# Kernel optimization log

Hardware: AMD Instinct MI355X
Metric: run time of the kernel (lower is better)

Reference implementation:

```python
import jax, jax.numpy as jnp
import numpy as np

B, S, D, L = 64, 512, 768, 2


def setup_inputs() -> dict:
    key = jax.random.key(0)
    ks = jax.random.split(key, 8)
    sc = 1.0 / np.sqrt(D)
    sequence_output = jax.random.normal(ks[0], (B, S, D), dtype=jnp.float32)
    sot_positions = jax.random.randint(ks[1], (B, S), 0, 2, dtype=jnp.int32)
    # guarantee every sample has at least one selected token (torch nonzero-gather assumes this)
    sot_positions = sot_positions.at[:, 0].set(1)
    W_ih = jax.random.uniform(ks[2], (3 * D, D), jnp.float32, -sc, sc)
    W_hh = jax.random.uniform(ks[3], (3 * D, D), jnp.float32, -sc, sc)
    b_ih = jax.random.uniform(ks[4], (3 * D,), jnp.float32, -sc, sc)
    b_hh = jax.random.uniform(ks[5], (3 * D,), jnp.float32, -sc, sc)
    W_cls = jax.random.uniform(ks[6], (L, D), jnp.float32, -sc, sc)
    b_cls = jax.random.uniform(ks[7], (L,), jnp.float32, -sc, sc)
    return {"sequence_output": sequence_output, "sot_positions": sot_positions,
            "W_ih": W_ih, "W_hh": W_hh, "b_ih": b_ih, "b_hh": b_hh,
            "W_cls": W_cls, "b_cls": b_cls}


def _masked_gru_last(seq, mask, W_ih, W_hh, b_ih, b_hh):
    """Equivalent to: per sample, gather tokens where mask!=0, run a 1-layer GRU
    over that subsequence, return the final hidden state. Vectorized as a scan
    over time that freezes the hidden state at non-selected positions."""
    # precompute input projections for all timesteps: [B,S,3D]
    x_proj = jnp.einsum('bsd,ed->bse', seq, W_ih) + b_ih
    xs = (jnp.swapaxes(x_proj, 0, 1), jnp.swapaxes(mask, 0, 1))  # time-major
    h0 = jnp.zeros((seq.shape[0], W_hh.shape[1]), seq.dtype)

    def step(h, inp):
        xp, m = inp  # xp: [B,3D], m: [B]
        hp = h @ W_hh.T + b_hh  # [B,3D]
        xr, xz, xn = jnp.split(xp, 3, axis=-1)
        hr, hz, hn = jnp.split(hp, 3, axis=-1)
        r = jax.nn.sigmoid(xr + hr)
        z = jax.nn.sigmoid(xz + hz)
        n = jnp.tanh(xn + r * hn)
        h_new = (1.0 - z) * n + z * h
        h = jnp.where((m != 0)[:, None], h_new, h)
        return h, None

    h_last, _ = jax.lax.scan(step, h0, xs)
    return h_last  # [B,D]


def reference(sequence_output, sot_positions, W_ih, W_hh, b_ih, b_hh, W_cls, b_cls):
    match_vec = _masked_gru_last(sequence_output, sot_positions, W_ih, W_hh, b_ih, b_hh)
    # dropout is identity at eval time
    logits = match_vec @ W_cls.T + b_cls  # [B,L]
    return jax.nn.softmax(logits, axis=1)
```

## Files before the change

### kernel.cpp

```cpp
#include <hip/hip_runtime.h>
#include <hip/hip_bf16.h>


#define NB 64
#define NS 512
#define ND 768
#define TD 2304
#define NM 24

typedef __attribute__((ext_vector_type(4))) float f32x4;
typedef __attribute__((ext_vector_type(8))) short bf16x8;
typedef __attribute__((ext_vector_type(4))) unsigned int u32x4;

__device__ inline unsigned short f2bf(float f) {
  union { float f; unsigned u; } a; a.f = f;
  unsigned r = a.u + 0x7fff + ((a.u >> 16) & 1);
  return (unsigned short)(r >> 16);
}
__device__ inline float bf2f(unsigned short s) {
  union { unsigned u; float f; } a; a.u = ((unsigned)s) << 16;
  return a.f;
}

__device__ inline void load2_flag(const int* p0, const int* p1, int& a, int& b) {
  asm volatile("global_load_dword %0, %2, off sc0 sc1\n\t"
               "global_load_dword %1, %3, off sc0 sc1\n\t"
               "s_waitcnt vmcnt(0)"
               : "=&v"(a), "=&v"(b) : "v"(p0), "v"(p1) : "memory");
}
__device__ inline void store_flag(int* p, int v) {
  asm volatile("global_store_dword %0, %1, off sc0 sc1"
               :: "v"(p), "v"(v) : "memory");
}
__device__ inline void store_h16(void* p, u32x4 v) {
  asm volatile("global_store_dwordx4 %0, %1, off sc0 sc1"
               :: "v"(p), "v"(v) : "memory");
}
__device__ inline void load2_h16(const void* p0, const void* p1,
                                 u32x4& a, u32x4& b) {
  asm volatile("global_load_dwordx4 %0, %2, off sc0 sc1\n\t"
               "global_load_dwordx4 %1, %3, off sc0 sc1\n\t"
               "s_waitcnt vmcnt(0)"
               : "=&v"(a), "=&v"(b) : "v"(p0), "v"(p1) : "memory");
}
__device__ inline void waitcnt_vm0() {
  asm volatile("s_waitcnt vmcnt(0)" ::: "memory");
}

__global__ void cvt_f32_bf16(const float* __restrict__ in,
                             unsigned short* __restrict__ out, int n) {
  int i = (blockIdx.x * blockDim.x + threadIdx.x) * 4;
  int stride = gridDim.x * blockDim.x * 4;
  for (; i < n; i += stride) {
    float4 v = *(const float4*)(in + i);
    ushort4 o;
    o.x = f2bf(v.x); o.y = f2bf(v.y); o.z = f2bf(v.z); o.w = f2bf(v.w);
    *(ushort4*)(out + i) = o;
  }
}

__global__ void compact_pos(const int* __restrict__ sot,
                            int* __restrict__ pos, int* __restrict__ ctrl) {
  int b = blockIdx.x, t = threadIdx.x;
  int m = (sot[b * NS + t] != 0) ? 1 : 0;
  unsigned long long ball = __ballot(m);
  int wid = t >> 6, lane = t & 63;
  __shared__ int wcnt[8];
  int prefix = __popcll(ball & ((1ull << lane) - 1ull));
  if (lane == 63) wcnt[wid] = __popcll(ball);
  __syncthreads();
  int base = 0;
  for (int w = 0; w < wid; ++w) base += wcnt[w];
  if (m) pos[b * NS + base + prefix] = t;
  if (t == 511) {
    int total = base + wcnt[7];
    ctrl[b] = total;
    atomicMax(&ctrl[64], total);
  }
}

#define BM 128
#define BN 256
__global__ __launch_bounds__(256) void gemm_xg(
    const float* __restrict__ seq,
    const int* __restrict__ pos,
    const int* __restrict__ ctrl,
    const unsigned short* __restrict__ Bg,
    const float* __restrict__ bias,
    unsigned short* __restrict__ C) {
  const int cntmax = ctrl[64];
  const int m0 = blockIdx.x * BM;
  if (m0 >= cntmax * 64) return;
  const int n0 = blockIdx.y * BN;
  __shared__ unsigned short lA[BM * 64];
  __shared__ unsigned short lB[BN * 64];
  const int tid = threadIdx.x;
  const int wid = tid >> 6, lane = tid & 63;
  const int wm = (wid & 1) * 64, wn = (wid >> 1) * 128;

  f32x4 acc[4][8];
#pragma unroll
  for (int i = 0; i < 4; ++i)
#pragma unroll
    for (int j = 0; j < 8; ++j) { f32x4 z = {0.f,0.f,0.f,0.f}; acc[i][j] = z; }

  for (int kt = 0; kt < 12; ++kt) {
    __syncthreads();
#pragma unroll
    for (int c = 0; c < 4; ++c) {
      int idx = c * 256 + tid;
      int r = idx >> 3, ch = idx & 7;
      int gm = m0 + r, ks = gm >> 6, ss = gm & 63;
      float4 v0 = {0,0,0,0}, v1 = {0,0,0,0};
      if (ks < ctrl[ss]) {
        int t = pos[ss * NS + ks];
        const float* src = seq + ((size_t)ss * NS + t) * ND + kt * 64 + ch * 8;
        v0 = *(const float4*)src;
        v1 = *(const float4*)(src + 4);
      }
      uint4 o;
      o.x = f2bf(v0.x) | ((unsigned)f2bf(v0.y) << 16);
      o.y = f2bf(v0.z) | ((unsigned)f2bf(v0.w) << 16);
      o.z = f2bf(v1.x) | ((unsigned)f2bf(v1.y) << 16);
      o.w = f2bf(v1.z) | ((unsigned)f2bf(v1.w) << 16);
      *(uint4*)((char*)lA + r * 128 + ((ch * 16) ^ ((r & 7) << 4))) = o;
    }
#pragma unroll
    for (int c = 0; c < 8; ++c) {
      int idx = c * 256 + tid;
      int r = idx >> 3, ch = idx & 7;
      uint4 v = *(const uint4*)(Bg + (size_t)(n0 + r) * ND + kt * 64 + ch * 8);
      *(uint4*)((char*)lB + r * 128 + ((ch * 16) ^ ((r & 7) << 4))) = v;
    }
    __syncthreads();
#pragma unroll
    for (int kk = 0; kk < 2; ++kk) {
      bf16x8 af[4], bfr[8];
      int kb = kk * 64 + (lane >> 4) * 16;
#pragma unroll
      for (int i = 0; i < 4; ++i) {
        int rowA = wm + i * 16 + (lane & 15);
        af[i] = *(const bf16x8*)((const char*)lA + rowA * 128 + (kb ^ ((rowA & 7) << 4)));
      }
#pragma unroll
      for (int i = 0; i < 8; ++i) {
        int rowB = wn + i * 16 + (lane & 15);
        bfr[i] = *(const bf16x8*)((const char*)lB + rowB * 128 + (kb ^ ((rowB & 7) << 4)));
      }
#pragma unroll
      for (int mi = 0; mi < 4; ++mi)
#pragma unroll
        for (int ni = 0; ni < 8; ++ni)
          acc[mi][ni] = __builtin_amdgcn_mfma_f32_16x16x32_bf16(
              af[mi], bfr[ni], acc[mi][ni], 0, 0, 0);
    }
  }
#pragma unroll
  for (int mi = 0; mi < 4; ++mi)
#pragma unroll
    for (int ni = 0; ni < 8; ++ni) {
      int col = n0 + wn + ni * 16 + (lane & 15);
      float bv = bias[col];
#pragma unroll
      for (int j = 0; j < 4; ++j) {
        int row = m0 + wm + mi * 16 + (lane >> 4) * 4 + j;
        C[(size_t)row * TD + col] = f2bf(acc[mi][ni][j] + bv);
      }
    }
}

__global__ __launch_bounds__(384) void rnn_gang(
    const unsigned short* __restrict__ xg,
    const unsigned short* __restrict__ whhb,
    const float* __restrict__ bhh,
    const int* __restrict__ ctrl,
    int* __restrict__ canary,
    unsigned short* __restrict__ Hb,
    const float* __restrict__ wcls,
    float* __restrict__ partial) {
  const int g  = blockIdx.x & 7;
  const int m  = blockIdx.x >> 3;
  const int d0 = m * 32;
  const int t  = threadIdx.x;
  const int w  = t >> 6;
  const int lane = t & 63;
  const int c  = lane & 15;
  const int kg = lane >> 4;

  __shared__ __align__(16) char Hl[8 * 1536];
  __shared__ __align__(16) float hp[8][100];
  __shared__ __align__(16) unsigned short hstage[256];

  const int lr = w * 16 + c;
  const int grow = (lr >> 5) * ND + d0 + (lr & 31);
  bf16x8 afr[24];
#pragma unroll
  for (int kt = 0; kt < 24; ++kt)
    afr[kt] = *(const bf16x8*)(whhb + (size_t)grow * ND + kt * 32 + kg * 8);

  const int s  = (t >> 5) & 7;
  const int d  = t & 31;
  const int sg = g * 8 + s;
  float br = 0.f, bz = 0.f, bn = 0.f, h = 0.f;
  int cnt_s = 0;
  if (t < 256) {
    br = bhh[d0 + d]; bz = bhh[ND + d0 + d]; bn = bhh[2 * ND + d0 + d];
    cnt_s = ctrl[sg];
  }
  int Kg = 0;
  for (int i = 0; i < 8; ++i) Kg = max(Kg, ctrl[g * 8 + i]);
  unsigned short* HG = Hb + (size_t)g * 8 * ND;
  int* CG = canary + g * 256;

  const int i0 = t, i1 = t + 384;
  const int r0 = i0 / 96, c0 = i0 - r0 * 96;
  const int r1 = i1 / 96, c1 = i1 - r1 * 96;
  const int* cy0 = CG + (c0 >> 2) * 8 + r0;
  const int* cy1 = CG + (c1 >> 2) * 8 + r1;

  if (t < 32) {
    u32x4 z = {0u, 0u, 0u, 0u};
    store_h16(HG + (t >> 2) * ND + d0 + (t & 3) * 8, z);
  }
  waitcnt_vm0();
  if (t < 8) store_flag(&CG[m * 8 + t], 1);

  float xr = 0.f, xz = 0.f, xn = 0.f;
  if (t < 256) {
    const unsigned short* xrow = xg + (size_t)sg * TD + d0 + d;
    xr = bf2f(xrow[0]); xz = bf2f(xrow[ND]); xn = bf2f(xrow[2 * ND]);
  }

  int dead = 0;
  for (int k = 0; k < Kg; ++k) {
    {
      const unsigned tk = (unsigned)(k + 1);
      if (!dead) {
        int spins = 0, v0, v1;
        for (;;) {
          load2_flag(cy0, cy1, v0, v1);
          if ((unsigned)v0 >= tk && (unsigned)v1 >= tk) break;
          if (++spins > (1 << 20)) { dead = 1; break; }
        }
      }
      u32x4 a0, a1;
      load2_h16(HG + r0 * ND + c0 * 8, HG + r1 * ND + c1 * 8, a0, a1);
      *(u32x4*)(Hl + r0 * 1536 + ((c0 * 16) ^ ((r0 & 7) << 4))) = a0;
      *(u32x4*)(Hl + r1 * 1536 + ((c1 * 16) ^ ((r1 & 7) << 4))) = a1;
    }
    float nxr = 0.f, nxz = 0.f, nxn = 0.f;
    if (t < 256) {
      int kn = (k + 1 < Kg) ? k + 1 : k;
      const unsigned short* xrow = xg + ((size_t)kn * 64 + sg) * TD + d0 + d;
      nxr = bf2f(xrow[0]); nxz = bf2f(xrow[ND]); nxn = bf2f(xrow[2 * ND]);
    }
    __syncthreads();
    f32x4 acc = {0.f, 0.f, 0.f, 0.f};
#pragma unroll
    for (int kt = 0; kt < 24; ++kt) {
      bf16x8 bfr = *(const bf16x8*)(Hl + (c & 7) * 1536 +
                    ((kt * 64 + kg * 16) ^ ((c & 7) << 4)));
      acc = __builtin_amdgcn_mfma_f32_16x16x32_bf16(afr[kt], bfr, acc, 0, 0, 0);
    }
    if (c < 8) *(f32x4*)&hp[c][w * 16 + kg * 4] = acc;
    __syncthreads();
    if (t < 256) {
      float ar = hp[s][d]      + br;
      float az = hp[s][32 + d] + bz;
      float an = hp[s][64 + d] + bn;
      float r  = 1.f / (1.f + __expf(-(xr + ar)));
      float z  = 1.f / (1.f + __expf(-(xz + az)));
      float nn = tanhf(xn + r * an);
      float hn = (1.f - z) * nn + z * h;
      if (k < cnt_s) h = hn;
      hstage[(s << 5) | d] = f2bf(h);
    }
    xr = nxr; xz = nxz; xn = nxn;
    __syncthreads();
    if (t < 32) {
      u32x4 q = *(const u32x4*)((const char*)hstage + (t >> 2) * 64 + (t & 3) * 16);
      store_h16(HG + (t >> 2) * ND + d0 + (t & 3) * 8, q);
    }
    waitcnt_vm0();
    if (t < 8) store_flag(&CG[m * 8 + t], k + 2);
  }

  if (t < 256) {
    float p0 = h * wcls[d0 + d];
    float p1 = h * wcls[ND + d0 + d];
#pragma unroll
    for (int off = 16; off; off >>= 1) {
      p0 += __shfl_xor(p0, off);
      p1 += __shfl_xor(p1, off);
    }
    if (d == 0) {
      partial[(size_t)(m * 64 + sg) * 2]     = p0;
      partial[(size_t)(m * 64 + sg) * 2 + 1] = p1;
    }
  }
}

__global__ void finalize(const float* __restrict__ partial,
                         const float* __restrict__ bcls,
                         float* __restrict__ out) {
  int s = threadIdx.x;
  float l0 = bcls[0], l1 = bcls[1];
  for (int m = 0; m < NM; ++m) {
    l0 += partial[(size_t)(m * 64 + s) * 2];
    l1 += partial[(size_t)(m * 64 + s) * 2 + 1];
  }
  float mx = fmaxf(l0, l1);
  float e0 = __expf(l0 - mx), e1 = __expf(l1 - mx);
  float inv = 1.f / (e0 + e1);
  out[2 * s]     = e0 * inv;
  out[2 * s + 1] = e1 * inv;
}

extern "C" void kernel_launch(void* const* d_in, const int* in_sizes, int n_in,
                              void* d_out, int out_size, void* d_ws, size_t ws_size,
                              hipStream_t stream) {
  const float* seq  = (const float*)d_in[0];
  const int*   sot  = (const int*)d_in[1];
  const float* Wih  = (const float*)d_in[2];
  const float* Whh  = (const float*)d_in[3];
  const float* bih  = (const float*)d_in[4];
  const float* bhh  = (const float*)d_in[5];
  const float* Wcls = (const float*)d_in[6];
  const float* bcls = (const float*)d_in[7];
  float* out = (float*)d_out;

  char* ws = (char*)d_ws;
  unsigned short* xg   = (unsigned short*)(ws);
  unsigned short* wihb = (unsigned short*)(ws + 150994944);
  unsigned short* whhb = (unsigned short*)(ws + 154533888);
  int*            pos  = (int*)(ws + 158072832);
  int*            ctrl = (int*)(ws + 158203904);
  int*            cn   = (int*)(ws + 158204416);
  unsigned short* Hb   = (unsigned short*)(ws + 158212608);
  float*          part = (float*)(ws + 158310912);

  cvt_f32_bf16<<<1728, 256, 0, stream>>>(Wih, wihb, TD * ND);
  cvt_f32_bf16<<<1728, 256, 0, stream>>>(Whh, whhb, TD * ND);
  hipMemsetAsync(ctrl, 0, 512 + 8192, stream);
  compact_pos<<<NB, NS, 0, stream>>>(sot, pos, ctrl);
  gemm_xg<<<dim3(NB * NS / BM, TD / BN), 256, 0, stream>>>(seq, pos, ctrl, wihb, bih, xg);
  rnn_gang<<<192, 384, 0, stream>>>(xg, whhb, bhh, ctrl, cn, Hb, Wcls, part);
  finalize<<<1, 64, 0, stream>>>(part, bcls, out);
}
```

Baseline: 1.142 ms.

## Replace flag-based cross-block handoff with tagged hidden-state words and double buffering

Each hidden value is now published as a 32-bit word that packs the bf16 value with a step tag. Consumers spin directly on the data words rather than on separate canary flags, and the buffer is double-buffered by step parity. This removes the extra __syncthreads, the LDS staging, the store-then-waitcnt-then-flag sequence and the separate flag polling on every step of the recurrence, which shortens the critical path between blocks. In exchange each step moves twice as many bytes, needs a larger buffer with a memset, and uses a bounded spin that may silently continue on timeout.

```diff
diff --git a/kernel.cpp b/kernel.cpp
--- a/kernel.cpp
+++ b/kernel.cpp
@@ -7,6 +7,7 @@
 #define ND 768
 #define TD 2304
 #define NM 24
+#define HXPAR 49152
 
 typedef __attribute__((ext_vector_type(4))) float f32x4;
 typedef __attribute__((ext_vector_type(8))) short bf16x8;
@@ -22,29 +23,21 @@
   return a.f;
 }
 
-__device__ inline void load2_flag(const int* p0, const int* p1, int& a, int& b) {
-  asm volatile("global_load_dword %0, %2, off sc0 sc1\n\t"
-               "global_load_dword %1, %3, off sc0 sc1\n\t"
-               "s_waitcnt vmcnt(0)"
-               : "=&v"(a), "=&v"(b) : "v"(p0), "v"(p1) : "memory");
-}
-__device__ inline void store_flag(int* p, int v) {
+__device__ inline void load4_tag(const unsigned* p,
+                                 u32x4& a, u32x4& b, u32x4& c, u32x4& d) {
+  asm volatile(
+      "global_load_dwordx4 %0, %4, off sc0 sc1\n\t"
+      "global_load_dwordx4 %1, %5, off sc0 sc1\n\t"
+      "global_load_dwordx4 %2, %6, off sc0 sc1\n\t"
+      "global_load_dwordx4 %3, %7, off sc0 sc1\n\t"
+      "s_waitcnt vmcnt(0)"
+      : "=&v"(a), "=&v"(b), "=&v"(c), "=&v"(d)
+      : "v"(p), "v"(p + 4), "v"(p + 8), "v"(p + 12)
+      : "memory");
+}
+__device__ inline void store_tag(unsigned* p, unsigned v) {
   asm volatile("global_store_dword %0, %1, off sc0 sc1"
                :: "v"(p), "v"(v) : "memory");
-}
-__device__ inline void store_h16(void* p, u32x4 v) {
-  asm volatile("global_store_dwordx4 %0, %1, off sc0 sc1"
-               :: "v"(p), "v"(v) : "memory");
-}
-__device__ inline void load2_h16(const void* p0, const void* p1,
-                                 u32x4& a, u32x4& b) {
-  asm volatile("global_load_dwordx4 %0, %2, off sc0 sc1\n\t"
-               "global_load_dwordx4 %1, %3, off sc0 sc1\n\t"
-               "s_waitcnt vmcnt(0)"
-               : "=&v"(a), "=&v"(b) : "v"(p0), "v"(p1) : "memory");
-}
-__device__ inline void waitcnt_vm0() {
-  asm volatile("s_waitcnt vmcnt(0)" ::: "memory");
 }
 
 __global__ void cvt_f32_bf16(const float* __restrict__ in,
@@ -174,8 +167,7 @@
     const unsigned short* __restrict__ whhb,
     const float* __restrict__ bhh,
     const int* __restrict__ ctrl,
-    int* __restrict__ canary,
-    unsigned short* __restrict__ Hb,
+    unsigned* __restrict__ Hx,
     const float* __restrict__ wcls,
     float* __restrict__ partial) {
   const int g  = blockIdx.x & 7;
@@ -189,7 +181,6 @@
 
   __shared__ __align__(16) char Hl[8 * 1536];
   __shared__ __align__(16) float hp[8][100];
-  __shared__ __align__(16) unsigned short hstage[256];
 
   const int lr = w * 16 + c;
   const int grow = (lr >> 5) * ND + d0 + (lr & 31);
@@ -209,21 +200,17 @@
   }
   int Kg = 0;
   for (int i = 0; i < 8; ++i) Kg = max(Kg, ctrl[g * 8 + i]);
-  unsigned short* HG = Hb + (size_t)g * 8 * ND;
-  int* CG = canary + g * 256;
-
-  const int i0 = t, i1 = t + 384;
-  const int r0 = i0 / 96, c0 = i0 - r0 * 96;
-  const int r1 = i1 / 96, c1 = i1 - r1 * 96;
-  const int* cy0 = CG + (c0 >> 2) * 8 + r0;
-  const int* cy1 = CG + (c1 >> 2) * 8 + r1;
-
-  if (t < 32) {
-    u32x4 z = {0u, 0u, 0u, 0u};
-    store_h16(HG + (t >> 2) * ND + d0 + (t & 3) * 8, z);
-  }
-  waitcnt_vm0();
-  if (t < 8) store_flag(&CG[m * 8 + t], 1);
+
+  const int sr   = t / 48;
+  const int sc16 = (t - sr * 48) * 16;
+  const unsigned* sbase = Hx + (size_t)(g * 8 + sr) * ND + sc16;
+  char* ldst = Hl + sr * 1536;
+  const int sb0 = (sc16 * 2)      ^ ((sr & 7) << 4);
+  const int sb1 = (sc16 * 2 + 16) ^ ((sr & 7) << 4);
+
+  unsigned* mypub = (t < 256) ? (Hx + (size_t)sg * ND + d0 + d) : Hx;
+
+  if (t < 256) store_tag(mypub, 1u << 16);
 
   float xr = 0.f, xz = 0.f, xn = 0.f;
   if (t < 256) {
@@ -231,27 +218,40 @@
     xr = bf2f(xrow[0]); xz = bf2f(xrow[ND]); xn = bf2f(xrow[2 * ND]);
   }
 
-  int dead = 0;
   for (int k = 0; k < Kg; ++k) {
     {
       const unsigned tk = (unsigned)(k + 1);
-      if (!dead) {
-        int spins = 0, v0, v1;
-        for (;;) {
-          load2_flag(cy0, cy1, v0, v1);
-          if ((unsigned)v0 >= tk && (unsigned)v1 >= tk) break;
-          if (++spins > (1 << 20)) { dead = 1; break; }
-        }
-      }
-      u32x4 a0, a1;
-      load2_h16(HG + r0 * ND + c0 * 8, HG + r1 * ND + c1 * 8, a0, a1);
-      *(u32x4*)(Hl + r0 * 1536 + ((c0 * 16) ^ ((r0 & 7) << 4))) = a0;
-      *(u32x4*)(Hl + r1 * 1536 + ((c1 * 16) ^ ((r1 & 7) << 4))) = a1;
+      const unsigned* src = sbase + (size_t)(k & 1) * HXPAR;
+      u32x4 q0, q1, q2, q3;
+      int spins = 0;
+      for (;;) {
+        load4_tag(src, q0, q1, q2, q3);
+        unsigned mn = q0[0] >> 16;
+        mn = min(mn, q0[1] >> 16); mn = min(mn, q0[2] >> 16); mn = min(mn, q0[3] >> 16);
+        mn = min(mn, q1[0] >> 16); mn = min(mn, q1[1] >> 16); mn = min(mn, q1[2] >> 16);
+        mn = min(mn, q1[3] >> 16);
+        mn = min(mn, q2[0] >> 16); mn = min(mn, q2[1] >> 16); mn = min(mn, q2[2] >> 16);
+        mn = min(mn, q2[3] >> 16);
+        mn = min(mn, q3[0] >> 16); mn = min(mn, q3[1] >> 16); mn = min(mn, q3[2] >> 16);
+        mn = min(mn, q3[3] >> 16);
+        if (mn >= tk) break;
+        if (++spins > (1 << 17)) break;
+      }
+      unsigned p0 = (q0[0] & 0xffffu) | (q0[1] << 16);
+      unsigned p1 = (q0[2] & 0xffffu) | (q0[3] << 16);
+      unsigned p2 = (q1[0] & 0xffffu) | (q1[1] << 16);
+      unsigned p3 = (q1[2] & 0xffffu) | (q1[3] << 16);
+      unsigned p4 = (q2[0] & 0xffffu) | (q2[1] << 16);
+      unsigned p5 = (q2[2] & 0xffffu) | (q2[3] << 16);
+      unsigned p6 = (q3[0] & 0xffffu) | (q3[1] << 16);
+      unsigned p7 = (q3[2] & 0xffffu) | (q3[3] << 16);
+      u32x4 A = {p0, p1, p2, p3}, B = {p4, p5, p6, p7};
+      *(u32x4*)(ldst + sb0) = A;
+      *(u32x4*)(ldst + sb1) = B;
     }
     float nxr = 0.f, nxz = 0.f, nxn = 0.f;
-    if (t < 256) {
-      int kn = (k + 1 < Kg) ? k + 1 : k;
-      const unsigned short* xrow = xg + ((size_t)kn * 64 + sg) * TD + d0 + d;
+    if (t < 256 && k + 1 < Kg) {
+      const unsigned short* xrow = xg + ((size_t)(k + 1) * 64 + sg) * TD + d0 + d;
       nxr = bf2f(xrow[0]); nxz = bf2f(xrow[ND]); nxn = bf2f(xrow[2 * ND]);
     }
     __syncthreads();
@@ -273,16 +273,10 @@
       float nn = tanhf(xn + r * an);
       float hn = (1.f - z) * nn + z * h;
       if (k < cnt_s) h = hn;
-      hstage[(s << 5) | d] = f2bf(h);
+      unsigned pv = (unsigned)f2bf(h) | ((unsigned)(k + 2) << 16);
+      store_tag(mypub + (size_t)((k + 1) & 1) * HXPAR, pv);
     }
     xr = nxr; xz = nxz; xn = nxn;
-    __syncthreads();
-    if (t < 32) {
-      u32x4 q = *(const u32x4*)((const char*)hstage + (t >> 2) * 64 + (t & 3) * 16);
-      store_h16(HG + (t >> 2) * ND + d0 + (t & 3) * 8, q);
-    }
-    waitcnt_vm0();
-    if (t < 8) store_flag(&CG[m * 8 + t], k + 2);
   }
 
   if (t < 256) {
@@ -335,15 +329,15 @@
   unsigned short* whhb = (unsigned short*)(ws + 154533888);
   int*            pos  = (int*)(ws + 158072832);
   int*            ctrl = (int*)(ws + 158203904);
-  int*            cn   = (int*)(ws + 158204416);
-  unsigned short* Hb   = (unsigned short*)(ws + 158212608);
-  float*          part = (float*)(ws + 158310912);
+  unsigned*       Hx   = (unsigned*)(ws + 158204416);
+  float*          part = (float*)(ws + 159777280);
 
   cvt_f32_bf16<<<1728, 256, 0, stream>>>(Wih, wihb, TD * ND);
   cvt_f32_bf16<<<1728, 256, 0, stream>>>(Whh, whhb, TD * ND);
-  hipMemsetAsync(ctrl, 0, 512 + 8192, stream);
+  hipMemsetAsync(ctrl, 0, 512, stream);
+  hipMemsetAsync(Hx, 0, 2 * 64 * ND * 4, stream);
   compact_pos<<<NB, NS, 0, stream>>>(sot, pos, ctrl);
   gemm_xg<<<dim3(NB * NS / BM, TD / BN), 256, 0, stream>>>(seq, pos, ctrl, wihb, bih, xg);
-  rnn_gang<<<192, 384, 0, stream>>>(xg, whhb, bhh, ctrl, cn, Hb, Wcls, part);
+  rnn_gang<<<192, 384, 0, stream>>>(xg, whhb, bhh, ctrl, Hx, Wcls, part);
   finalize<<<1, 64, 0, stream>>>(part, bcls, out);
 }
```

After: 1.255 ms. +9.9%, slower.
